# Optimization experiments

Measured on AMD Instinct MI355X. Metric: run time of the kernel, lower is better.

Reference implementation:

```python
import jax, jax.numpy as jnp
import numpy as np
import math

B, L, D, H = 2, 4096, 1024, 16
DH = D // H


def _build_table(seq_len):
    # Faithful port of build_hierarchical_index_lookup_table (static, host-side).
    assert seq_len & (seq_len - 1) == 0
    levels = int(math.log2(seq_len))
    max_valid = 2 * seq_len - 3
    idx = np.full((seq_len, levels), -1, dtype=np.int64)
    cm = np.zeros((seq_len, levels), dtype=bool)
    for n in range(seq_len):
        c = n
        for lvl in range(levels):
            if lvl == 0:
                nxt = c ^ 1
                pair = c
            else:
                nxt = (c // 2 + seq_len) ^ 1
                pair = c // 2 + seq_len
            if nxt > max_valid:
                break
            if pair < nxt:
                cm[n, lvl] = True
            idx[n, lvl] = nxt
            c = nxt
    return idx, cm


def setup_inputs() -> dict:
    rng = jax.random.key(0)
    ks = jax.random.split(rng, 8)
    s = 0.02  # init scale for weights
    idx, cm = _build_table(L)
    return {
        "query": jax.random.normal(ks[0], (B, L, D), jnp.float32),
        "key": jax.random.normal(ks[1], (B, L, D), jnp.float32),
        "value": jax.random.normal(ks[2], (B, L, D), jnp.float32),
        "Wq": jax.random.normal(ks[3], (D, D), jnp.float32) * s,
        "Wk": jax.random.normal(ks[4], (D, D), jnp.float32) * s,
        "Wv": jax.random.normal(ks[5], (D, D), jnp.float32) * s,
        "Wo": jax.random.normal(ks[6], (D, D), jnp.float32) * s,
        "bo": jax.random.normal(ks[7], (D,), jnp.float32) * s,
        "idx_table": jnp.asarray(idx),        # [L, log2(L)] int64
        "causal_mask": jnp.asarray(cm),       # [L, log2(L)] bool
    }


def reference(query, key, value, Wq, Wk, Wv, Wo, bo, idx_table, causal_mask):
    Bq, Lq, Dm = query.shape
    scale = 1.0 / math.sqrt(DH)

    def heads(x, W):  # nn.Linear (no bias) + split heads -> [B,H,L,Dh]
        return (x @ W.T).reshape(Bq, Lq, H, DH).transpose(0, 2, 1, 3)

    Q = heads(query, Wq)
    K = heads(key, Wk)
    V = heads(value, Wv)

    # Build binary-tree hierarchy. Pair weights come from softmax of ZERO
    # logits (Q_parent starts as zeros in the source), so w0 = w1 = 0.5 exactly.
    Ks, Vs = [K], [V]
    while Ks[-1].shape[2] > 1:
        k, v = Ks[-1], Vs[-1]
        Lc = k.shape[2]
        k2 = k.reshape(Bq, H, Lc // 2, 2, DH)
        v2 = v.reshape(Bq, H, Lc // 2, 2, DH)
        Ks.append(0.5 * (k2[:, :, :, 0] + k2[:, :, :, 1]))
        Vs.append(v2[:, :, :, 0] + v2[:, :, :, 1])
    flatK = jnp.concatenate(Ks, axis=2)  # [B,H,2L-1,Dh]
    flatV = jnp.concatenate(Vs, axis=2)

    # Gather neighbor nodes across levels: [B,H,L,levels,Dh]
    nk = flatK[:, :, idx_table]
    nv = flatV[:, :, idx_table]

    self_logits = jnp.einsum('bhnd,bhnd->bhn', Q, K) * scale
    nbr_logits = jnp.einsum('bhld,bhlnd->bhln', Q, nk) * scale
    nbr_logits = jnp.where(causal_mask[None, None], -jnp.inf, nbr_logits)

    all_logits = jnp.concatenate([self_logits[..., None], nbr_logits], axis=-1)
    w = jax.nn.softmax(all_logits, axis=-1)           # [B,H,L,1+levels]
    all_v = jnp.concatenate([V[:, :, :, None, :], nv], axis=3)
    out = jnp.einsum('bhln,bhlnd->bhld', w, all_v)    # [B,H,L,Dh]
    out = out.transpose(0, 2, 1, 3).reshape(Bq, Lq, Dm)
    return out @ Wo.T + bo
```

## Files before the change

### kernel.cpp

```cpp
#include <hip/hip_runtime.h>
#include <cstdint>
#include <cstddef>


typedef __bf16 bf16;
typedef __bf16 bf16x8 __attribute__((ext_vector_type(8)));
typedef __bf16 bf16x4 __attribute__((ext_vector_type(4)));
typedef float  f32x4  __attribute__((ext_vector_type(4)));

#define L_SEQ  4096
#define NFLAT  8192

__device__ __forceinline__ int off_l(int l) { return 8192 - (8192 >> l); }

__device__ __forceinline__ void glds16(const bf16* g, bf16* l) {
  __builtin_amdgcn_global_load_lds(
      (const __attribute__((address_space(1))) unsigned int*)g,
      (__attribute__((address_space(3))) unsigned int*)l, 16, 0, 0);
}

__global__ __launch_bounds__(256) void cvt3_kernel(
    const float* __restrict__ a, const float* __restrict__ b, const float* __restrict__ c,
    bf16* __restrict__ x, bf16* __restrict__ y, bf16* __restrict__ z) {
  const int s = blockIdx.y;
  const float* src = (s == 0) ? a : (s == 1) ? b : c;
  bf16*        dst = (s == 0) ? x : (s == 1) ? y : z;
  const int i = blockIdx.x * 256 + threadIdx.x;
  const float4 v = ((const float4*)src)[i];
  bf16x4 o;
  o[0] = (bf16)v.x; o[1] = (bf16)v.y; o[2] = (bf16)v.z; o[3] = (bf16)v.w;
  *(bf16x4*)(dst + (size_t)i * 4) = o;
}

__global__ __launch_bounds__(256) void cvt4_kernel(
    const float* __restrict__ a, const float* __restrict__ b,
    const float* __restrict__ c, const float* __restrict__ d,
    bf16* __restrict__ x, bf16* __restrict__ y, bf16* __restrict__ z, bf16* __restrict__ w) {
  const int s = blockIdx.y;
  const float* src = (s == 0) ? a : (s == 1) ? b : (s == 2) ? c : d;
  bf16*        dst = (s == 0) ? x : (s == 1) ? y : (s == 2) ? z : w;
  const int i = blockIdx.x * 256 + threadIdx.x;
  const float4 v = ((const float4*)src)[i];
  bf16x4 o;
  o[0] = (bf16)v.x; o[1] = (bf16)v.y; o[2] = (bf16)v.z; o[3] = (bf16)v.w;
  *(bf16x4*)(dst + (size_t)i * 4) = o;
}

__device__ __forceinline__ void gemm_core(const bf16* __restrict__ A,
                                          const bf16* __restrict__ W,
                                          int tm, int tn, bf16* As, bf16* Bs,
                                          f32x4 (&acc)[4][4]) {
  const int tid  = threadIdx.x;
  const int wave = tid >> 6, lane = tid & 63;
  const int wm = (wave >> 1) * 64, wn = (wave & 1) * 64;
  for (int k0 = 0; k0 < 1024; k0 += 32) {
#pragma unroll
    for (int c = 0; c < 2; c++) {
      const int base = c * 4096 + wave * 1024;
      const int off  = base + lane * 16;
      const int row  = off >> 6;
      const int kk   = (off & 63) >> 1;
      glds16(A + (size_t)(tm * 128 + row) * 1024 + k0 + kk, As + (base >> 1));
      glds16(W + (size_t)(tn * 128 + row) * 1024 + k0 + kk, Bs + (base >> 1));
    }
    __syncthreads();
    bf16x8 af[4], bfr[4];
#pragma unroll
    for (int i = 0; i < 4; i++) {
      af[i]  = *(const bf16x8*)&As[(wm + i * 16 + (lane & 15)) * 32 + (lane >> 4) * 8];
      bfr[i] = *(const bf16x8*)&Bs[(wn + i * 16 + (lane & 15)) * 32 + (lane >> 4) * 8];
    }
#pragma unroll
    for (int i = 0; i < 4; i++)
#pragma unroll
      for (int j = 0; j < 4; j++)
        acc[i][j] = __builtin_amdgcn_mfma_f32_16x16x32_bf16(af[i], bfr[j], acc[i][j], 0, 0, 0);
    __syncthreads();
  }
}

__global__ __launch_bounds__(256) void gemm_qkv_kernel(
    const bf16* __restrict__ qx, const bf16* __restrict__ kx, const bf16* __restrict__ vx,
    const bf16* __restrict__ wq, const bf16* __restrict__ wk, const bf16* __restrict__ wv,
    bf16* __restrict__ Qb, bf16* __restrict__ fK, bf16* __restrict__ fV) {
  __shared__ __align__(16) bf16 As[128 * 32];
  __shared__ __align__(16) bf16 Bs[128 * 32];
  const int z = blockIdx.y;
  const bf16* A = (z == 0) ? qx : (z == 1) ? kx : vx;
  const bf16* W = (z == 0) ? wq : (z == 1) ? wk : wv;
  bf16* D       = (z == 0) ? Qb : (z == 1) ? fK : fV;
  const int lstr = (z == 0) ? L_SEQ : NFLAT;
  const int tm = blockIdx.x & 63, tn = blockIdx.x >> 6;
  f32x4 acc[4][4] = {};
  gemm_core(A, W, tm, tn, As, Bs, acc);
  const int lane = threadIdx.x & 63, wave = threadIdx.x >> 6;
  const int m0 = tm * 128 + (wave >> 1) * 64 + (lane >> 4) * 4;
  const int n0 = tn * 128 + (wave & 1) * 64 + (lane & 15);
#pragma unroll
  for (int i = 0; i < 4; i++)
#pragma unroll
    for (int j = 0; j < 4; j++)
#pragma unroll
      for (int r = 0; r < 4; r++) {
        const int m = m0 + i * 16 + r;
        const int n = n0 + j * 16;
        const int b = m >> 12, l = m & 4095;
        const int h = n >> 6,  dh = n & 63;
        D[((size_t)(b * 16 + h) * lstr + l) * 64 + dh] = (bf16)acc[i][j][r];
      }
}

__global__ __launch_bounds__(256) void gemm_out_kernel(
    const bf16* __restrict__ Ob, const bf16* __restrict__ wo,
    const float* __restrict__ bo, float* __restrict__ out) {
  __shared__ __align__(16) bf16 As[128 * 32];
  __shared__ __align__(16) bf16 Bs[128 * 32];
  const int tm = blockIdx.x & 63, tn = blockIdx.x >> 6;
  f32x4 acc[4][4] = {};
  gemm_core(Ob, wo, tm, tn, As, Bs, acc);
  const int lane = threadIdx.x & 63, wave = threadIdx.x >> 6;
  const int m0 = tm * 128 + (wave >> 1) * 64 + (lane >> 4) * 4;
  const int n0 = tn * 128 + (wave & 1) * 64 + (lane & 15);
#pragma unroll
  for (int i = 0; i < 4; i++)
#pragma unroll
    for (int j = 0; j < 4; j++)
#pragma unroll
      for (int r = 0; r < 4; r++) {
        const int m = m0 + i * 16 + r;
        const int n = n0 + j * 16;
        out[(size_t)m * 1024 + n] = acc[i][j][r] + bo[n];
      }
}

__global__ __launch_bounds__(64) void tree_l16(bf16* __restrict__ fK, bf16* __restrict__ fV) {
  __shared__ __align__(16) bf16 Kl[64 * 64];
  __shared__ __align__(16) bf16 Vl[64 * 64];
  const int g = blockIdx.x, bh = blockIdx.y;
  const int lane = threadIdx.x;
  const size_t fb = (size_t)bh * NFLAT * 64;
  const size_t leafbase = fb + (size_t)g * 64 * 64;
#pragma unroll
  for (int it = 0; it < 8; it++) {
    glds16(fK + leafbase + it * 512 + lane * 8, Kl + it * 512);
    glds16(fV + leafbase + it * 512 + lane * 8, Vl + it * 512);
  }
  asm volatile("s_waitcnt vmcnt(0)" ::: "memory");
  __syncthreads();

  float pk[7], pv[7];
#pragma unroll
  for (int i = 0; i < 64; i++) {
    float ck = (float)Kl[i * 64 + lane];
    float cv = (float)Vl[i * 64 + lane];
#pragma unroll
    for (int l = 1; l <= 6; l++) {
      if (((i + 1) & ((1 << l) - 1)) != 0) { pk[l] = ck; pv[l] = cv; break; }
      ck += pk[l]; cv += pv[l];
      const int j = (g * 64 + i) >> l;
      fK[fb + (size_t)(off_l(l) + j) * 64 + lane] = (bf16)(ck * (1.0f / (1 << l)));
      fV[fb + (size_t)(off_l(l) + j) * 64 + lane] = (bf16)cv;
    }
  }
}

__global__ __launch_bounds__(64) void tree_l712(bf16* __restrict__ fK, bf16* __restrict__ fV) {
  __shared__ float Ks[64 * 64];
  __shared__ float Vs[64 * 64];
  const int bh = blockIdx.x, d = threadIdx.x;
  const size_t fb = (size_t)bh * NFLAT * 64;
#pragma unroll 8
  for (int i = 0; i < 64; i++) {
    Ks[i * 64 + d] = (float)fK[fb + (size_t)(8064 + i) * 64 + d];
    Vs[i * 64 + d] = (float)fV[fb + (size_t)(8064 + i) * 64 + d];
  }
#pragma unroll
  for (int l = 7; l <= 12; l++) {
    const int cnt = 4096 >> l;
    for (int j = 0; j < cnt; j++) {
      const float k = (Ks[(2 * j) * 64 + d] + Ks[(2 * j + 1) * 64 + d]) * 0.5f;
      const float v =  Vs[(2 * j) * 64 + d] + Vs[(2 * j + 1) * 64 + d];
      Ks[j * 64 + d] = k;
      Vs[j * 64 + d] = v;
      fK[fb + (size_t)(off_l(l) + j) * 64 + d] = (bf16)k;
      fV[fb + (size_t)(off_l(l) + j) * 64 + d] = (bf16)v;
    }
  }
}

__global__ __launch_bounds__(64) void attn_kernel(
    const bf16* __restrict__ Qb, const bf16* __restrict__ fK,
    const bf16* __restrict__ fV, bf16* __restrict__ Ob) {
  __shared__ __align__(16) unsigned short Kl[132 * 64];
  __shared__ __align__(16) unsigned short Vl[132 * 64];
  const int t0  = blockIdx.x * 64;
  const int bh  = blockIdx.y;
  const int tid = threadIdx.x;
  const size_t fb = (size_t)bh * NFLAT * 64;

  for (int u = tid; u < 132 * 8; u += 64) {
    const int r = u >> 3, c = u & 7;
    int flat;
    if      (r < 64)  flat = t0 + r;
    else if (r < 96)  flat = 4096 + (t0 >> 1) + (r - 64);
    else if (r < 112) flat = 6144 + (t0 >> 2) + (r - 96);
    else if (r < 120) flat = 7168 + (t0 >> 3) + (r - 112);
    else if (r < 124) flat = 7680 + (t0 >> 4) + (r - 120);
    else if (r < 126) flat = 7936 + (t0 >> 5) + (r - 124);
    else { const int l = r - 120; flat = (8192 - (8192 >> l) + (t0 >> l)) ^ 1; }
    const int cc = c ^ (r & 7);
    const uint4 kk = *(const uint4*)((const char*)(fK + fb + (size_t)flat * 64) + c * 16);
    const uint4 vv = *(const uint4*)((const char*)(fV + fb + (size_t)flat * 64) + c * 16);
    *(uint4*)((char*)Kl + r * 128 + cc * 16) = kk;
    *(uint4*)((char*)Vl + r * 128 + cc * 16) = vv;
  }
  __syncthreads();

  const int n = t0 + tid;
  int rows[13];
  rows[0] = tid;
#pragma unroll
  for (int l = 0; l < 12; l++) {
    int r;
    if (l == 0)      r = tid ^ 1;
    else if (l <= 5) r = (128 - (128 >> l)) + (((n >> l) ^ 1) - (t0 >> l));
    else             r = 126 + (l - 6);
    rows[l + 1] = r;
  }

  float q[64];
  const bf16* Qr = Qb + ((size_t)bh * L_SEQ + n) * 64;
#pragma unroll
  for (int c = 0; c < 8; c++) {
    bf16x8 v = *(const bf16x8*)(Qr + c * 8);
#pragma unroll
    for (int j = 0; j < 8; j++) q[c * 8 + j] = (float)v[j];
  }

  float lg[13];
#pragma unroll
  for (int v = 0; v < 13; v++) {
    const int r = rows[v];
    float a = 0.f;
#pragma unroll
    for (int c = 0; c < 8; c++) {
      const int cc = c ^ (r & 7);
      const bf16x8 kv = *(const bf16x8*)((const char*)Kl + r * 128 + cc * 16);
#pragma unroll
      for (int j = 0; j < 8; j++) a += q[c * 8 + j] * (float)kv[j];
    }
    lg[v] = a * 0.125f;
  }
#pragma unroll
  for (int v = 1; v < 13; v++)
    if (!((n >> (v - 1)) & 1)) lg[v] = -1e30f;

  float mx = lg[0];
#pragma unroll
  for (int v = 1; v < 13; v++) mx = fmaxf(mx, lg[v]);
  float w[13], s = 0.f;
#pragma unroll
  for (int v = 0; v < 13; v++) { w[v] = __expf(lg[v] - mx); s += w[v]; }
  const float inv = 1.0f / s;

  float o[64];
#pragma unroll
  for (int d = 0; d < 64; d++) o[d] = 0.f;
#pragma unroll
  for (int v = 0; v < 13; v++) {
    const int r = rows[v];
    const float wv = w[v];
#pragma unroll
    for (int c = 0; c < 8; c++) {
      const int cc = c ^ (r & 7);
      const bf16x8 vv = *(const bf16x8*)((const char*)Vl + r * 128 + cc * 16);
#pragma unroll
      for (int j = 0; j < 8; j++) o[c * 8 + j] += wv * (float)vv[j];
    }
  }

  bf16* Or = Ob + ((size_t)(bh >> 4) * L_SEQ + n) * 1024 + (size_t)(bh & 15) * 64;
#pragma unroll
  for (int c = 0; c < 8; c++) {
    bf16x8 ov;
#pragma unroll
    for (int j = 0; j < 8; j++) ov[j] = (bf16)(o[c * 8 + j] * inv);
    *(bf16x8*)(Or + c * 8) = ov;
  }
}

extern "C" void kernel_launch(void* const* d_in, const int* in_sizes, int n_in,
                              void* d_out, int out_size, void* d_ws, size_t ws_size,
                              hipStream_t stream) {
  const float* query = (const float*)d_in[0];
  const float* key   = (const float*)d_in[1];
  const float* value = (const float*)d_in[2];
  const float* Wq    = (const float*)d_in[3];
  const float* Wk    = (const float*)d_in[4];
  const float* Wv    = (const float*)d_in[5];
  const float* Wo    = (const float*)d_in[6];
  const float* bo    = (const float*)d_in[7];
  float* out = (float*)d_out;

  char* ws = (char*)d_ws;
  size_t off = 0;
  auto take = [&](size_t bytes) -> void* {
    void* p = ws + off;
    off += (bytes + 255) & ~(size_t)255;
    return p;
  };
  const size_t XB = (size_t)8192 * 1024 * 2;
  const size_t WB = (size_t)1024 * 1024 * 2;
  bf16* qx  = (bf16*)take(XB);
  bf16* kx  = (bf16*)take(XB);
  bf16* vx  = (bf16*)take(XB);
  bf16* wqx = (bf16*)take(WB);
  bf16* wkx = (bf16*)take(WB);
  bf16* wvx = (bf16*)take(WB);
  bf16* wox = (bf16*)take(WB);
  bf16* Qb  = (bf16*)take((size_t)32 * L_SEQ * 64 * 2);
  bf16* fK  = (bf16*)take((size_t)32 * NFLAT * 64 * 2);
  bf16* fV  = (bf16*)take((size_t)32 * NFLAT * 64 * 2);
  bf16* Ob  = qx;
  (void)in_sizes; (void)n_in; (void)out_size; (void)ws_size;

  cvt3_kernel<<<dim3(8192, 3), 256, 0, stream>>>(query, key, value, qx, kx, vx);
  cvt4_kernel<<<dim3(1024, 4), 256, 0, stream>>>(Wq, Wk, Wv, Wo, wqx, wkx, wvx, wox);

  gemm_qkv_kernel<<<dim3(512, 3), 256, 0, stream>>>(qx, kx, vx, wqx, wkx, wvx, Qb, fK, fV);

  tree_l16 <<<dim3(64, 32), 64, 0, stream>>>(fK, fV);
  tree_l712<<<32, 64, 0, stream>>>(fK, fV);

  attn_kernel<<<dim3(64, 32), 64, 0, stream>>>(Qb, fK, fV, Ob);

  gemm_out_kernel<<<512, 256, 0, stream>>>(Ob, wox, bo, out);
}
```

Baseline: 179.1 us.

## Rewrite GEMMs with 8-wave 128x256 tiles, double-buffered swizzled LDS pipeline

Replaces the 4-wave 128x128 single-buffered GEMM core with an 8-wave kernel on 128x256 tiles and K-step 64. Global-to-LDS loads for the next K tile go into a second buffer while MFMAs run on the current one. LDS addresses are XOR-swizzled to avoid bank conflicts, and raw barriers plus s_setprio sit around the MFMA bursts. This targets the exposed load latency and the barrier overhead of the old GEMM, which are the main cost in the projection matmuls. The price is more LDS per block (96 KB), hand-tuned waitcnt logic that is fragile, and fewer blocks per launch.

```diff
diff --git a/kernel.cpp b/kernel.cpp
--- a/kernel.cpp
+++ b/kernel.cpp
@@ -17,6 +17,16 @@
   __builtin_amdgcn_global_load_lds(
       (const __attribute__((address_space(1))) unsigned int*)g,
       (__attribute__((address_space(3))) unsigned int*)l, 16, 0, 0);
+}
+
+#define MEMFENCE asm volatile("" ::: "memory")
+__device__ __forceinline__ void barrier_raw() {
+  MEMFENCE; __builtin_amdgcn_s_barrier(); MEMFENCE;
+}
+
+__device__ __forceinline__ int swz(int b) { return b ^ (((b >> 9) & 1) << 5); }
+__device__ __forceinline__ int la(int row, int col) {
+  return ((((row >> 4) << 1) + (col >> 5)) << 10) + ((row & 15) << 6) + ((col & 31) << 1);
 }
 
 __global__ __launch_bounds__(256) void cvt3_kernel(
@@ -46,56 +56,102 @@
   *(bf16x4*)(dst + (size_t)i * 4) = o;
 }
 
-__device__ __forceinline__ void gemm_core(const bf16* __restrict__ A,
-                                          const bf16* __restrict__ W,
-                                          int tm, int tn, bf16* As, bf16* Bs,
-                                          f32x4 (&acc)[4][4]) {
+__device__ __forceinline__ void stage_tile(const bf16* __restrict__ A,
+                                           const bf16* __restrict__ W,
+                                           int tm, int tn, int k0,
+                                           bf16* AsP, bf16* BsP, int wid, int lane) {
+#pragma unroll
+  for (int i = 0; i < 2; i++) {
+    const int d  = i * 8192 + wid * 1024 + lane * 16;
+    const int lb = swz(d);
+    const int row = ((lb >> 10) >> 1) * 16 + ((lb >> 6) & 15);
+    const int col = ((lb >> 10) & 1) * 32 + ((lb & 63) >> 1);
+    glds16(A + (size_t)(tm * 128 + row) * 1024 + k0 + col, AsP + i * 4096 + wid * 512);
+  }
+#pragma unroll
+  for (int i = 0; i < 4; i++) {
+    const int d  = i * 8192 + wid * 1024 + lane * 16;
+    const int lb = swz(d);
+    const int row = ((lb >> 10) >> 1) * 16 + ((lb >> 6) & 15);
+    const int col = ((lb >> 10) & 1) * 32 + ((lb & 63) >> 1);
+    glds16(W + (size_t)(tn * 256 + row) * 1024 + k0 + col, BsP + i * 4096 + wid * 512);
+  }
+}
+
+__device__ __forceinline__ void gemm8_core(const bf16* __restrict__ A,
+                                           const bf16* __restrict__ W,
+                                           int tm, int tn,
+                                           bf16 (*As)[128 * 64], bf16 (*Bs)[256 * 64],
+                                           f32x4 (&acc)[4][4]) {
   const int tid  = threadIdx.x;
-  const int wave = tid >> 6, lane = tid & 63;
-  const int wm = (wave >> 1) * 64, wn = (wave & 1) * 64;
-  for (int k0 = 0; k0 < 1024; k0 += 32) {
-#pragma unroll
-    for (int c = 0; c < 2; c++) {
-      const int base = c * 4096 + wave * 1024;
-      const int off  = base + lane * 16;
-      const int row  = off >> 6;
-      const int kk   = (off & 63) >> 1;
-      glds16(A + (size_t)(tm * 128 + row) * 1024 + k0 + kk, As + (base >> 1));
-      glds16(W + (size_t)(tn * 128 + row) * 1024 + k0 + kk, Bs + (base >> 1));
-    }
-    __syncthreads();
-    bf16x8 af[4], bfr[4];
-#pragma unroll
-    for (int i = 0; i < 4; i++) {
-      af[i]  = *(const bf16x8*)&As[(wm + i * 16 + (lane & 15)) * 32 + (lane >> 4) * 8];
-      bfr[i] = *(const bf16x8*)&Bs[(wn + i * 16 + (lane & 15)) * 32 + (lane >> 4) * 8];
-    }
-#pragma unroll
-    for (int i = 0; i < 4; i++)
-#pragma unroll
-      for (int j = 0; j < 4; j++)
-        acc[i][j] = __builtin_amdgcn_mfma_f32_16x16x32_bf16(af[i], bfr[j], acc[i][j], 0, 0, 0);
-    __syncthreads();
-  }
-}
-
-__global__ __launch_bounds__(256) void gemm_qkv_kernel(
+  const int wid  = tid >> 6, lane = tid & 63;
+  const int wm2  = wid >> 2, wn4 = wid & 3;
+  const int laneR  = lane & 15;
+  const int laneC8 = (lane >> 4) * 8;
+
+  stage_tile(A, W, tm, tn, 0,  As[0], Bs[0], wid, lane);
+  stage_tile(A, W, tm, tn, 64, As[1], Bs[1], wid, lane);
+  asm volatile("s_waitcnt vmcnt(6)" ::: "memory");
+  barrier_raw();
+
+  for (int t = 0; t < 16; ++t) {
+    const int p = t & 1;
+    const char* Ab = (const char*)As[p];
+    const char* Bb = (const char*)Bs[p];
+#pragma unroll
+    for (int q = 0; q < 2; ++q) {
+      bf16x8 af[2][2], bfr[4][2];
+#pragma unroll
+      for (int f = 0; f < 2; f++)
+#pragma unroll
+        for (int ks = 0; ks < 2; ks++) {
+          const int row = wm2 * 64 + (2 * q + f) * 16 + laneR;
+          af[f][ks] = *(const bf16x8*)(Ab + swz(la(row, ks * 32 + laneC8)));
+        }
+#pragma unroll
+      for (int f = 0; f < 4; f++)
+#pragma unroll
+        for (int ks = 0; ks < 2; ks++) {
+          const int row = wn4 * 64 + f * 16 + laneR;
+          bfr[f][ks] = *(const bf16x8*)(Bb + swz(la(row, ks * 32 + laneC8)));
+        }
+      if (q == 0 && t >= 1 && t < 15)
+        stage_tile(A, W, tm, tn, (t + 1) << 6, As[p ^ 1], Bs[p ^ 1], wid, lane);
+      barrier_raw();
+      __builtin_amdgcn_s_setprio(1);
+#pragma unroll
+      for (int f = 0; f < 2; f++)
+#pragma unroll
+        for (int j = 0; j < 4; j++)
+#pragma unroll
+          for (int ks = 0; ks < 2; ks++)
+            acc[2 * q + f][j] = __builtin_amdgcn_mfma_f32_16x16x32_bf16(
+                af[f][ks], bfr[j][ks], acc[2 * q + f][j], 0, 0, 0);
+      __builtin_amdgcn_s_setprio(0);
+      if (q == 1 && t < 15)
+        asm volatile("s_waitcnt vmcnt(0)" ::: "memory");
+      barrier_raw();
+    }
+  }
+}
+
+__global__ __launch_bounds__(512, 2) void gemm8_qkv_kernel(
     const bf16* __restrict__ qx, const bf16* __restrict__ kx, const bf16* __restrict__ vx,
     const bf16* __restrict__ wq, const bf16* __restrict__ wk, const bf16* __restrict__ wv,
     bf16* __restrict__ Qb, bf16* __restrict__ fK, bf16* __restrict__ fV) {
-  __shared__ __align__(16) bf16 As[128 * 32];
-  __shared__ __align__(16) bf16 Bs[128 * 32];
+  __shared__ __align__(16) bf16 As[2][128 * 64];
+  __shared__ __align__(16) bf16 Bs[2][256 * 64];
   const int z = blockIdx.y;
   const bf16* A = (z == 0) ? qx : (z == 1) ? kx : vx;
   const bf16* W = (z == 0) ? wq : (z == 1) ? wk : wv;
   bf16* D       = (z == 0) ? Qb : (z == 1) ? fK : fV;
   const int lstr = (z == 0) ? L_SEQ : NFLAT;
-  const int tm = blockIdx.x & 63, tn = blockIdx.x >> 6;
+  const int tm = blockIdx.x >> 2, tn = blockIdx.x & 3;
   f32x4 acc[4][4] = {};
-  gemm_core(A, W, tm, tn, As, Bs, acc);
-  const int lane = threadIdx.x & 63, wave = threadIdx.x >> 6;
-  const int m0 = tm * 128 + (wave >> 1) * 64 + (lane >> 4) * 4;
-  const int n0 = tn * 128 + (wave & 1) * 64 + (lane & 15);
+  gemm8_core(A, W, tm, tn, As, Bs, acc);
+  const int lane = threadIdx.x & 63, wid = threadIdx.x >> 6;
+  const int m0 = tm * 128 + (wid >> 2) * 64 + (lane >> 4) * 4;
+  const int n0 = tn * 256 + (wid & 3) * 64 + (lane & 15);
 #pragma unroll
   for (int i = 0; i < 4; i++)
 #pragma unroll
@@ -110,17 +166,17 @@
       }
 }
 
-__global__ __launch_bounds__(256) void gemm_out_kernel(
+__global__ __launch_bounds__(512, 2) void gemm8_out_kernel(
     const bf16* __restrict__ Ob, const bf16* __restrict__ wo,
     const float* __restrict__ bo, float* __restrict__ out) {
-  __shared__ __align__(16) bf16 As[128 * 32];
-  __shared__ __align__(16) bf16 Bs[128 * 32];
-  const int tm = blockIdx.x & 63, tn = blockIdx.x >> 6;
+  __shared__ __align__(16) bf16 As[2][128 * 64];
+  __shared__ __align__(16) bf16 Bs[2][256 * 64];
+  const int tm = blockIdx.x >> 2, tn = blockIdx.x & 3;
   f32x4 acc[4][4] = {};
-  gemm_core(Ob, wo, tm, tn, As, Bs, acc);
-  const int lane = threadIdx.x & 63, wave = threadIdx.x >> 6;
-  const int m0 = tm * 128 + (wave >> 1) * 64 + (lane >> 4) * 4;
-  const int n0 = tn * 128 + (wave & 1) * 64 + (lane & 15);
+  gemm8_core(Ob, wo, tm, tn, As, Bs, acc);
+  const int lane = threadIdx.x & 63, wid = threadIdx.x >> 6;
+  const int m0 = tm * 128 + (wid >> 2) * 64 + (lane >> 4) * 4;
+  const int n0 = tn * 256 + (wid & 3) * 64 + (lane & 15);
 #pragma unroll
   for (int i = 0; i < 4; i++)
 #pragma unroll
@@ -327,12 +383,12 @@
   cvt3_kernel<<<dim3(8192, 3), 256, 0, stream>>>(query, key, value, qx, kx, vx);
   cvt4_kernel<<<dim3(1024, 4), 256, 0, stream>>>(Wq, Wk, Wv, Wo, wqx, wkx, wvx, wox);
 
-  gemm_qkv_kernel<<<dim3(512, 3), 256, 0, stream>>>(qx, kx, vx, wqx, wkx, wvx, Qb, fK, fV);
+  gemm8_qkv_kernel<<<dim3(256, 3), 512, 0, stream>>>(qx, kx, vx, wqx, wkx, wvx, Qb, fK, fV);
 
   tree_l16 <<<dim3(64, 32), 64, 0, stream>>>(fK, fV);
   tree_l712<<<32, 64, 0, stream>>>(fK, fV);
 
   attn_kernel<<<dim3(64, 32), 64, 0, stream>>>(Qb, fK, fV, Ob);
 
-  gemm_out_kernel<<<512, 256, 0, stream>>>(Ob, wox, bo, out);
-}
+  gemm8_out_kernel<<<256, 512, 0, stream>>>(Ob, wox, bo, out);
+}
```

Result: slower. 198.3 us (+10.7%).
